# Optimization experiments

Measured on AMD Instinct MI355X. Metric: run time of the kernel, lower is better.

Reference implementation:

```python
import jax, jax.numpy as jnp
import numpy as np

N_COMPONENTS = 8
N_DIMENSIONS = 16
N_POINTS = 500000


def setup_inputs() -> dict:
    key = jax.random.key(0)
    k1, k2, k3 = jax.random.split(key, 3)
    data = jax.random.normal(k1, (N_POINTS, N_DIMENSIONS), dtype=jnp.float32)
    logits = jnp.ones((N_COMPONENTS,), dtype=jnp.float32)
    means = jax.random.normal(k2, (N_COMPONENTS, N_DIMENSIONS), dtype=jnp.float32)
    scales = jax.random.normal(k3, (N_COMPONENTS, N_DIMENSIONS, N_DIMENSIONS), dtype=jnp.float32)
    return {"data": data, "logits": logits, "means": means, "scales": scales}


def _gmm_log_prob(data, logits, means, scales):
    # covariances = scales @ scales^T  -> [K, D, D]
    covs = jnp.einsum('kij,klj->kil', scales, scales)
    L = jnp.linalg.cholesky(covs)  # [K, D, D]
    # diff: [K, N, D]
    diff = data[None, :, :] - means[:, None, :]
    # solve L y = diff^T  -> y: [K, D, N]
    y = jax.scipy.linalg.solve_triangular(L, jnp.swapaxes(diff, 1, 2), lower=True)
    maha = jnp.sum(y * y, axis=1)  # [K, N]
    half_logdet = jnp.sum(jnp.log(jnp.diagonal(L, axis1=1, axis2=2)), axis=-1)  # [K]
    D = data.shape[-1]
    log2pi = jnp.float32(np.log(2.0 * np.pi))
    comp_lp = -0.5 * (maha + D * log2pi) - half_logdet[:, None]  # [K, N]
    mix_lp = jax.nn.log_softmax(logits)  # [K]
    return jax.scipy.special.logsumexp(mix_lp[:, None] + comp_lp, axis=0)  # [N]


def reference(data, logits, means, scales):
    return _gmm_log_prob(data, logits, means, scales)
```

## Files before the change

### kernel.cpp

```cpp
#include <hip/hip_runtime.h>
#include <math.h>

#define KC 8
#define DD 16
#define NPT 1
#define BLK 256

__global__ __launch_bounds__(128) void gmm_prep(
    const float* __restrict__ logits,
    const float* __restrict__ means,
    const float* __restrict__ scales,
    float* __restrict__ Aout,
    float* __restrict__ Bout,
    float* __restrict__ Cout)
{
    __shared__ float Ssh[KC][DD][DD];
    __shared__ float cov[KC][DD][DD + 1];
    __shared__ float Lsh[KC][DD][DD + 1];
    __shared__ float Ash[KC][DD][DD + 1];

    const int tid = threadIdx.x;
    const int k = tid >> 4;
    const int i = tid & 15;

    {
        const float4* s4 = (const float4*)scales;
        float4* d4 = (float4*)&Ssh[0][0][0];
        for (int t = tid; t < KC * DD * DD / 4; t += 128) d4[t] = s4[t];
    }
    __syncthreads();

    float si[DD];
#pragma unroll
    for (int d = 0; d < DD; ++d) si[d] = Ssh[k][i][d];
#pragma unroll
    for (int j = 0; j < DD; ++j) {
        float s = 0.f;
#pragma unroll
        for (int d = 0; d < DD; ++d) s = fmaf(si[d], Ssh[k][j][d], s);
        cov[k][i][j] = s;
    }
    __syncthreads();

    for (int j = 0; j < DD; ++j) {
        if (i == j) {
            float s = cov[k][j][j];
            for (int t = 0; t < j; ++t) s -= Lsh[k][j][t] * Lsh[k][j][t];
            Lsh[k][j][j] = sqrtf(s);
        }
        __syncthreads();
        if (i > j) {
            float s = cov[k][i][j];
            for (int t = 0; t < j; ++t) s -= Lsh[k][i][t] * Lsh[k][j][t];
            Lsh[k][i][j] = s / Lsh[k][j][j];
        }
        __syncthreads();
    }

    float xc[DD];
#pragma unroll
    for (int r = 0; r < DD; ++r) {
        float s = (r == i) ? 1.f : 0.f;
#pragma unroll
        for (int t = 0; t < DD; ++t) {
            if (t < r) s -= Lsh[k][r][t] * xc[t];
        }
        xc[r] = (r < i) ? 0.f : (s / Lsh[k][r][r]);
    }
#pragma unroll
    for (int r = 0; r < DD; ++r) Ash[k][r][i] = xc[r];
    __syncthreads();

    float bb = 0.f;
#pragma unroll
    for (int j = 0; j < DD; ++j) {
        float aij = Ash[k][i][j];
        Aout[(k * DD + i) * DD + j] = aij;
        bb = fmaf(aij, means[k * DD + j], bb);
    }
    Bout[k * DD + i] = bb;

    if (i == 0) {
        float mx = logits[0];
        for (int t = 1; t < KC; ++t) mx = fmaxf(mx, logits[t]);
        float se = 0.f;
        for (int t = 0; t < KC; ++t) se += expf(logits[t] - mx);
        float lse = mx + logf(se);
        float hl = 0.f;
        for (int r = 0; r < DD; ++r) hl += logf(Lsh[k][r][r]);
        const float log2pi = 1.8378770664093453f;
        Cout[k] = (logits[k] - lse) - hl - 0.5f * DD * log2pi;
    }
}

__global__ __launch_bounds__(BLK, 6) void gmm_lp(
    const float* __restrict__ data,
    const float* __restrict__ Ag,
    const float* __restrict__ Bg,
    const float* __restrict__ Cg,
    float* __restrict__ out, int N)
{
    const int id = blockIdx.x * BLK + threadIdx.x;
    const int cl = id < N ? id : N - 1;

    float x[DD];
    {
        const float4* xp = (const float4*)(data + (size_t)cl * DD);
#pragma unroll
        for (int q = 0; q < 4; ++q) {
            float4 v = xp[q];
            x[4 * q + 0] = v.x; x[4 * q + 1] = v.y;
            x[4 * q + 2] = v.z; x[4 * q + 3] = v.w;
        }
    }

    float mx = -1e30f, sum = 0.f;

#pragma unroll 1
    for (int k = 0; k < KC; ++k) {
        const float* Ak = Ag + k * DD * DD;
        float bk[DD];
        {
            const float4* b4 = (const float4*)(Bg + k * DD);
#pragma unroll
            for (int q = 0; q < 4; ++q) {
                float4 v = b4[q];
                bk[4 * q + 0] = v.x; bk[4 * q + 1] = v.y;
                bk[4 * q + 2] = v.z; bk[4 * q + 3] = v.w;
            }
        }
        const float ck = Cg[k];

        float maha = 0.f;
#pragma unroll
        for (int i = 0; i < DD; ++i) {
            float y = -bk[i];
#pragma unroll
            for (int g = 0; g <= i / 4; ++g) {
                float4 a = *(const float4*)(Ak + i * DD + 4 * g);
                y = fmaf(a.x, x[4 * g + 0], y);
                y = fmaf(a.y, x[4 * g + 1], y);
                y = fmaf(a.z, x[4 * g + 2], y);
                y = fmaf(a.w, x[4 * g + 3], y);
            }
            maha = fmaf(y, y, maha);
        }

        float lpk = fmaf(-0.5f, maha, ck);
        float nm = fmaxf(mx, lpk);
        sum = sum * __expf(mx - nm) + __expf(lpk - nm);
        mx = nm;
    }

    if (id < N) out[id] = mx + __logf(sum);
}

extern "C" void kernel_launch(void* const* d_in, const int* in_sizes, int n_in,
                              void* d_out, int out_size, void* d_ws, size_t ws_size,
                              hipStream_t stream) {
    const float* data   = (const float*)d_in[0];
    const float* logits = (const float*)d_in[1];
    const float* means  = (const float*)d_in[2];
    const float* scales = (const float*)d_in[3];
    float* out = (float*)d_out;
    const int N = in_sizes[0] / DD;

    float* A = (float*)d_ws;
    float* B = A + KC * DD * DD;
    float* C = B + KC * DD;

    gmm_prep<<<1, 128, 0, stream>>>(logits, means, scales, A, B, C);
    const int nblk = (N + BLK * NPT - 1) / (BLK * NPT);
    gmm_lp<<<nblk, BLK, 0, stream>>>(data, A, B, C, out, N);
}
```

Measured before the change: 110.6 us.

## Rewrite prep kernel Cholesky and covariance with wave shuffles instead of shared memory

The single-block prep kernel now computes the covariance, a right-looking Cholesky factorization, and the triangular inverse entirely in registers, exchanging values through 64-lane shuffles within each 16-thread group. This removes most shared-memory staging and the 32 block-wide barriers of the column-by-column Cholesky loop. It targets the serial latency of the tiny prep launch, which runs ahead of the main per-point kernel. It adds many shuffle instructions and more register pressure, and the Cholesky update order changes, which may perturb rounding slightly.

```diff
diff --git a/kernel.cpp b/kernel.cpp
--- a/kernel.cpp
+++ b/kernel.cpp
@@ -3,7 +3,6 @@
 
 #define KC 8
 #define DD 16
-#define NPT 1
 #define BLK 256
 
 __global__ __launch_bounds__(128) void gmm_prep(
@@ -14,47 +13,50 @@
     float* __restrict__ Bout,
     float* __restrict__ Cout)
 {
-    __shared__ float Ssh[KC][DD][DD];
-    __shared__ float cov[KC][DD][DD + 1];
-    __shared__ float Lsh[KC][DD][DD + 1];
-    __shared__ float Ash[KC][DD][DD + 1];
+    const int tid  = threadIdx.x;
+    const int k    = tid >> 4;
+    const int i    = tid & 15;
+    const int lane = tid & 63;
+    const int base = lane & 48;
 
-    const int tid = threadIdx.x;
-    const int k = tid >> 4;
-    const int i = tid & 15;
+    float srow[DD];
+    {
+        const float4* sp = (const float4*)(scales + (size_t)(k * DD + i) * DD);
+#pragma unroll
+        for (int q = 0; q < 4; ++q) {
+            float4 v = sp[q];
+            srow[4 * q + 0] = v.x; srow[4 * q + 1] = v.y;
+            srow[4 * q + 2] = v.z; srow[4 * q + 3] = v.w;
+        }
+    }
 
-    {
-        const float4* s4 = (const float4*)scales;
-        float4* d4 = (float4*)&Ssh[0][0][0];
-        for (int t = tid; t < KC * DD * DD / 4; t += 128) d4[t] = s4[t];
+    float a[DD];
+#pragma unroll
+    for (int j = 0; j < DD; ++j) a[j] = 0.f;
+#pragma unroll
+    for (int d = 0; d < DD; ++d) {
+        float sid = srow[d];
+#pragma unroll
+        for (int j = 0; j < DD; ++j) {
+            float sjd = __shfl(srow[d], base + j, 64);
+            a[j] = fmaf(sid, sjd, a[j]);
+        }
     }
-    __syncthreads();
 
-    float si[DD];
-#pragma unroll
-    for (int d = 0; d < DD; ++d) si[d] = Ssh[k][i][d];
+    float l[DD];
+    float hld = 0.f;
 #pragma unroll
     for (int j = 0; j < DD; ++j) {
-        float s = 0.f;
+        float ajj = __shfl(a[j], base + j, 64);
+        float ljj = sqrtf(ajj);
+        hld += logf(ljj);
+        float lij = (i < j) ? 0.f : (a[j] / ljj);
+        l[j] = lij;
 #pragma unroll
-        for (int d = 0; d < DD; ++d) s = fmaf(si[d], Ssh[k][j][d], s);
-        cov[k][i][j] = s;
-    }
-    __syncthreads();
-
-    for (int j = 0; j < DD; ++j) {
-        if (i == j) {
-            float s = cov[k][j][j];
-            for (int t = 0; t < j; ++t) s -= Lsh[k][j][t] * Lsh[k][j][t];
-            Lsh[k][j][j] = sqrtf(s);
+        for (int c = j + 1; c < DD; ++c) {
+            float lcj = __shfl(l[j], base + c, 64);
+            a[c] = fmaf(-lij, lcj, a[c]);
         }
-        __syncthreads();
-        if (i > j) {
-            float s = cov[k][i][j];
-            for (int t = 0; t < j; ++t) s -= Lsh[k][i][t] * Lsh[k][j][t];
-            Lsh[k][i][j] = s / Lsh[k][j][j];
-        }
-        __syncthreads();
     }
 
     float xc[DD];
@@ -63,10 +65,16 @@
         float s = (r == i) ? 1.f : 0.f;
 #pragma unroll
         for (int t = 0; t < DD; ++t) {
-            if (t < r) s -= Lsh[k][r][t] * xc[t];
+            if (t < r) {
+                float lrt = __shfl(l[t], base + r, 64);
+                s = fmaf(-lrt, xc[t], s);
+            }
         }
-        xc[r] = (r < i) ? 0.f : (s / Lsh[k][r][r]);
+        float lrr = __shfl(l[r], base + r, 64);
+        xc[r] = (r < i) ? 0.f : (s / lrr);
     }
+
+    __shared__ float Ash[KC][DD][DD + 1];
 #pragma unroll
     for (int r = 0; r < DD; ++r) Ash[k][r][i] = xc[r];
     __syncthreads();
@@ -86,10 +94,8 @@
         float se = 0.f;
         for (int t = 0; t < KC; ++t) se += expf(logits[t] - mx);
         float lse = mx + logf(se);
-        float hl = 0.f;
-        for (int r = 0; r < DD; ++r) hl += logf(Lsh[k][r][r]);
         const float log2pi = 1.8378770664093453f;
-        Cout[k] = (logits[k] - lse) - hl - 0.5f * DD * log2pi;
+        Cout[k] = (logits[k] - lse) - hld - 0.5f * DD * log2pi;
     }
 }
 
@@ -170,6 +176,6 @@
     float* C = B + KC * DD;
 
     gmm_prep<<<1, 128, 0, stream>>>(logits, means, scales, A, B, C);
-    const int nblk = (N + BLK * NPT - 1) / (BLK * NPT);
+    const int nblk = (N + BLK - 1) / BLK;
     gmm_lp<<<nblk, BLK, 0, stream>>>(data, A, B, C, out, N);
 }
```

Result: faster. 105.5 us (-4.5%).
